# Optimization experiments

Hardware: AMD Instinct MI355X
Metric: run time of the kernel (lower is better)

## Reference

```python
import jax, jax.numpy as jnp
import numpy as np

B, T, I, H, NCLS = 256, 784, 1, 110, 10


def setup_inputs() -> dict:
    key = jax.random.key(0)
    ks = jax.random.split(key, 10)
    s = 1.0 / np.sqrt(H)
    u = lambda k, shape: jax.random.uniform(k, shape, jnp.float32, -s, s)
    return {
        "x": jax.random.normal(ks[0], (B, T, I), jnp.float32),
        "W_ih": u(ks[1], (4 * H, I)),
        "W_hh": u(ks[2], (4 * H, H)),
        "b": u(ks[3], (4 * H,)),
        "W_p": u(ks[4], (1, H)),     # skip-gate readout of cell state
        "b_p": jnp.ones((1,), jnp.float32),  # bias init ~1 -> start by updating
        "h0": u(ks[5], (H,)),        # learned initial hidden (learn_init=True)
        "c0": u(ks[6], (H,)),        # learned initial cell
        "W_fc": u(ks[7], (NCLS, H)),
        "b_fc": u(ks[8], (NCLS,)),
    }


def _st_round(u):
    # straight-through binarization: round in fwd, identity grad in bwd
    return u + jax.lax.stop_gradient(jnp.round(u) - u)


def reference(x, W_ih, W_hh, b, W_p, b_p, h0, c0, W_fc, b_fc):
    Bsz = x.shape[0]
    Hh = h0.shape[0]
    xT = jnp.transpose(x, (1, 0, 2))  # [T, B, I] (the permute in Net.forward)
    h = jnp.broadcast_to(h0, (Bsz, Hh))
    c = jnp.broadcast_to(c0, (Bsz, Hh))
    u0 = jnp.ones((Bsz, 1), x.dtype)  # first step always updates

    def step(carry, xt):
        h, c, u = carry
        ub = _st_round(u)                                  # binary update gate [B,1]
        gates = xt @ W_ih.T + h @ W_hh.T + b               # [B, 4H]
        i, f, g, o = jnp.split(gates, 4, axis=-1)
        i = jax.nn.sigmoid(i)
        f = jax.nn.sigmoid(f)
        o = jax.nn.sigmoid(o)
        g = jnp.tanh(g)
        c_new = f * c + i * g
        h_new = o * jnp.tanh(c_new)
        c_n = ub * c_new + (1.0 - ub) * c                  # skip: keep old state
        h_n = ub * h_new + (1.0 - ub) * h
        du = jax.nn.sigmoid(c_n @ W_p.T + b_p)             # delta-u from cell [B,1]
        u_n = ub * du + (1.0 - ub) * (u + jnp.minimum(du, 1.0 - u))
        return (h_n, c_n, u_n), (h_n, ub)

    (h_last, _, _), (hs, ubs) = jax.lax.scan(step, (h, c, u0), xT)
    out = hs[-1] @ W_fc.T + b_fc                           # fc on last timestep
    total_u = jnp.sum(ubs)                                 # total number of updates
    return out, total_u[None]
```

## Files before the change

### kernel.cpp

```cpp
#include <hip/hip_runtime.h>
#include <stdint.h>


#define T784 784
#define H110 110
#define NT   512
#define NCLS 10
#define LOG2E 1.44269504088896340736f
#define WQS  (0.09535f / 127.0f)

typedef int v4i __attribute__((ext_vector_type(4)));

__device__ __forceinline__ float frcp(float x)  { return __builtin_amdgcn_rcpf(x); }
__device__ __forceinline__ float fexp2(float x) { return __builtin_amdgcn_exp2f(x); }

__device__ __forceinline__ float add_q1(float v) {
    float d; asm("v_add_f32_dpp %0, %1, %1 quad_perm:[1,0,3,2] row_mask:0xf bank_mask:0xf bound_ctrl:0"
                 : "=v"(d) : "v"(v)); return d;
}
__device__ __forceinline__ float add_q2(float v) {
    float d; asm("v_add_f32_dpp %0, %1, %1 quad_perm:[2,3,0,1] row_mask:0xf bank_mask:0xf bound_ctrl:0"
                 : "=v"(d) : "v"(v)); return d;
}
__device__ __forceinline__ float add_hm(float v) {
    float d; asm("v_add_f32_dpp %0, %1, %1 row_half_mirror row_mask:0xf bank_mask:0xf bound_ctrl:0"
                 : "=v"(d) : "v"(v)); return d;
}
__device__ __forceinline__ float add_rm(float v) {
    float d; asm("v_add_f32_dpp %0, %1, %1 row_mirror row_mask:0xf bank_mask:0xf bound_ctrl:0"
                 : "=v"(d) : "v"(v)); return d;
}
__device__ __forceinline__ float add_b15(float v) {
    float d; asm("v_add_f32_dpp %0, %1, %1 row_bcast:15 row_mask:0xf bank_mask:0xf bound_ctrl:0"
                 : "=v"(d) : "v"(v)); return d;
}
__device__ __forceinline__ float add_b31(float v) {
    float d; asm("v_add_f32_dpp %0, %1, %1 row_bcast:31 row_mask:0xf bank_mask:0xf bound_ctrl:0"
                 : "=v"(d) : "v"(v)); return d;
}
template <int L>
__device__ __forceinline__ float qbcast(float v) {
    float d;
    if (L == 0) asm("v_mov_b32_dpp %0, %1 quad_perm:[0,0,0,0] row_mask:0xf bank_mask:0xf bound_ctrl:0" : "=v"(d) : "v"(v));
    if (L == 1) asm("v_mov_b32_dpp %0, %1 quad_perm:[1,1,1,1] row_mask:0xf bank_mask:0xf bound_ctrl:0" : "=v"(d) : "v"(v));
    if (L == 2) asm("v_mov_b32_dpp %0, %1 quad_perm:[2,2,2,2] row_mask:0xf bank_mask:0xf bound_ctrl:0" : "=v"(d) : "v"(v));
    if (L == 3) asm("v_mov_b32_dpp %0, %1 quad_perm:[3,3,3,3] row_mask:0xf bank_mask:0xf bound_ctrl:0" : "=v"(d) : "v"(v));
    return d;
}

__device__ __forceinline__ int qpack(float f0, float f1, float f2, float f3) {
    const int q0 = (int)rintf(f0) & 0xFF;
    const int q1 = (int)rintf(f1) & 0xFF;
    const int q2 = (int)rintf(f2) & 0xFF;
    const int q3 = (int)rintf(f3) & 0xFF;
    return q0 | (q1 << 8) | (q2 << 16) | (q3 << 24);
}

__device__ __forceinline__ int vsel4(v4i a, bool r1, bool r2) {
    const int e01 = r1 ? a[1] : a[0];
    const int e23 = r1 ? a[3] : a[2];
    return r2 ? e23 : e01;
}

__global__ __launch_bounds__(NT, 2)
void skiplstm_kernel(const float* __restrict__ x,
                     const float* __restrict__ W_ih,
                     const float* __restrict__ W_hh,
                     const float* __restrict__ b,
                     const float* __restrict__ W_p,
                     const float* __restrict__ b_p,
                     const float* __restrict__ h0,
                     const float* __restrict__ c0,
                     const float* __restrict__ W_fc,
                     const float* __restrict__ b_fc,
                     float* __restrict__ out)
{
    __shared__ __align__(16) int s_h8[2][32];
    __shared__ float s_pbuf[256];
    __shared__ float s_x[T784];

    const int tid  = threadIdx.x;
    const int bb   = blockIdx.x;
    const int lane = tid & 63;
    const int wid  = tid >> 6;
    const int grp  = lane >> 4;
    const int c    = lane & 15;
    const int q    = tid >> 2;
    const int j    = tid & 3;
    const bool qact = (q < H110);

    const bool i1 = (lane & 4) != 0;
    const bool i2 = (lane & 8) != 0;

    const float qinv = 1.0f / WQS;
    const int  ut  = 16 * wid + c;
    const bool uta = (ut < H110);
    v4i aw[4][2];
    #pragma unroll
    for (int t = 0; t < 4; ++t) {
        const float* rp = W_hh + (t * H110 + ut) * H110;
        #pragma unroll
        for (int kk = 0; kk < 2; ++kk) {
            #pragma unroll
            for (int d = 0; d < 4; ++d) {
                float f[4];
                #pragma unroll
                for (int e = 0; e < 4; ++e) {
                    const int k = kk * 64 + grp * 16 + 4 * d + e;
                    f[e] = (uta && k < H110) ? rp[k] * qinv : 0.0f;
                }
                aw[t][kk][d] = qpack(f[0], f[1], f[2], f[3]);
            }
        }
    }

    const float gfac = (j == 2) ? (-2.0f * LOG2E) : (-LOG2E);
    const int   row  = j * H110 + q;
    const float bv = qact ? b[row]    * gfac : 0.0f;
    const float wv = qact ? W_ih[row] * gfac : 0.0f;
    const float scj = (WQS / 127.0f) * gfac;

    float creg = qact ? c0[q] : 0.0f;
    float hreg = qact ? h0[q] : 0.0f;
    const float wpn = qact ? (-LOG2E) * W_p[q] : 0.0f;
    const float bpn = (-LOG2E) * b_p[0];

    const float mulc = (j == 2) ? 2.0f : 1.0f;
    const float addc = (j == 2) ? -1.0f : 0.0f;

    const v4i z4 = {0, 0, 0, 0};

    for (int i = tid; i < 64;   i += NT) ((int*)s_h8)[i] = 0;
    for (int i = tid; i < 256;  i += NT) s_pbuf[i] = 0.0f;
    for (int i = tid; i < T784; i += NT) s_x[i] = x[bb * T784 + i];
    __syncthreads();
    if (tid < H110)
        ((int8_t*)s_h8[0])[tid] = (int8_t)__float2int_rn(h0[tid] * 127.0f);
    __syncthreads();

    float u_prev = 1.0f;
    int   cnt    = 0;

    auto step = [&](const int* hb, int* hn,
                    const float* pp, float* pn, int t, bool first) {
        const v4i bh0 = ((const v4i*)hb)[grp];
        const v4i bh1 = ((const v4i*)hb)[grp + 4];

        v4i acc0 = __builtin_amdgcn_mfma_i32_16x16x64_i8(aw[0][0], bh0, z4, 0, 0, 0);
        v4i acc1 = __builtin_amdgcn_mfma_i32_16x16x64_i8(aw[1][0], bh0, z4, 0, 0, 0);
        v4i acc2 = __builtin_amdgcn_mfma_i32_16x16x64_i8(aw[2][0], bh0, z4, 0, 0, 0);
        v4i acc3 = __builtin_amdgcn_mfma_i32_16x16x64_i8(aw[3][0], bh0, z4, 0, 0, 0);
        acc0 = __builtin_amdgcn_mfma_i32_16x16x64_i8(aw[0][1], bh1, acc0, 0, 0, 0);
        acc1 = __builtin_amdgcn_mfma_i32_16x16x64_i8(aw[1][1], bh1, acc1, 0, 0, 0);
        acc2 = __builtin_amdgcn_mfma_i32_16x16x64_i8(aw[2][1], bh1, acc2, 0, 0, 0);
        acc3 = __builtin_amdgcn_mfma_i32_16x16x64_i8(aw[3][1], bh1, acc3, 0, 0, 0);

        __builtin_amdgcn_sched_barrier(0);

        const float p0 = pp[lane], p1 = pp[lane + 64];
        const float xt = s_x[t];
        float u_now;
        if (first) {
            u_now = 1.0f;
        } else {
            float v = p0 + p1;
            v = add_q1(v); v = add_q2(v); v = add_hm(v);
            v = add_rm(v); v = add_b15(v); v = add_b31(v);
            const float tot = __int_as_float(
                __builtin_amdgcn_readlane(__float_as_int(v), 63));
            const float du = frcp(1.0f + fexp2(tot + bpn));
            u_now = (u_prev > 0.5f) ? du
                                    : (u_prev + fminf(du, 1.0f - u_prev));
        }
        const bool up = u_now > 0.5f;
        cnt += up ? 1 : 0;
        u_prev = u_now;

        const int e0 = vsel4(acc0, i1, i2);
        const int e1 = vsel4(acc1, i1, i2);
        const int e2 = vsel4(acc2, i1, i2);
        const int e3 = vsel4(acc3, i1, i2);
        const int e01 = (j & 1) ? e1 : e0;
        const int e23 = (j & 1) ? e3 : e2;
        const int ia  = (j & 2) ? e23 : e01;

        const float asel = fmaf((float)ia, scj, fmaf(xt, wv, bv));
        const float av = fmaf(mulc, frcp(1.0f + fexp2(asel)), addc);
        const float gi = qbcast<0>(av);
        const float gf = qbcast<1>(av);
        const float gg = qbcast<2>(av);
        const float go = qbcast<3>(av);

        const float cn = fmaf(gf, creg, gi * gg);
        const float th = fmaf(2.0f, frcp(1.0f + fexp2(cn * (-2.0f * LOG2E))), -1.0f);
        const float hn_ = go * th;
        creg = up ? cn : creg;
        hreg = up ? hn_ : hreg;
        if (qact && j == 0) {
            ((int8_t*)hn)[q] = (int8_t)__float2int_rn(hreg * 127.0f);
            pn[q] = creg * wpn;
        }
        __syncthreads();
    };

    int* const h0b = s_h8[0];
    int* const h1b = s_h8[1];
    float* const p0b = s_pbuf;
    float* const p1b = s_pbuf + 128;

    step(h0b, h1b, p0b, p1b, 0, true);
    step(h1b, h0b, p1b, p0b, 1, false);
    step(h0b, h1b, p0b, p1b, 2, false);
    step(h1b, h0b, p1b, p0b, 3, false);
    for (int t = 4; t < T784; t += 4) {
        step(h0b, h1b, p0b, p1b, t,     false);
        step(h1b, h0b, p1b, p0b, t + 1, false);
        step(h0b, h1b, p0b, p1b, t + 2, false);
        step(h1b, h0b, p1b, p0b, t + 3, false);
    }

    if (qact && j == 0) s_pbuf[q] = hreg;
    __syncthreads();
    if (tid < NCLS) {
        float acc = b_fc[tid];
        for (int k = 0; k < H110; ++k)
            acc = fmaf(s_pbuf[k], W_fc[tid * H110 + k], acc);
        out[bb * NCLS + tid] = acc;
    }
    if (tid == 0)
        atomicAdd(out + 256 * NCLS, (float)cnt);
}

__global__ void zero_tail_kernel(float* out) {
    if (threadIdx.x == 0) out[256 * NCLS] = 0.0f;
}

extern "C" void kernel_launch(void* const* d_in, const int* in_sizes, int n_in,
                              void* d_out, int out_size, void* d_ws, size_t ws_size,
                              hipStream_t stream) {
    const float* x    = (const float*)d_in[0];
    const float* W_ih = (const float*)d_in[1];
    const float* W_hh = (const float*)d_in[2];
    const float* b    = (const float*)d_in[3];
    const float* W_p  = (const float*)d_in[4];
    const float* b_p  = (const float*)d_in[5];
    const float* h0   = (const float*)d_in[6];
    const float* c0   = (const float*)d_in[7];
    const float* W_fc = (const float*)d_in[8];
    const float* b_fc = (const float*)d_in[9];
    float* out = (float*)d_out;

    zero_tail_kernel<<<1, 64, 0, stream>>>(out);
    skiplstm_kernel<<<256, NT, 0, stream>>>(x, W_ih, W_hh, b, W_p, b_p,
                                            h0, c0, W_fc, b_fc, out);
}
```

Before: 406.4 us.

## Halve block size so each thread computes two hidden units per step

Shrinks the workgroup from 8 to 4 waves, and each wave now issues MFMAs for two 64-row groups of hidden units (A and B halves). The gate activations, cell and hidden updates are duplicated per thread for the two units. The goal is to cut the per-timestep cost of the block-wide barrier and cross-wave coordination in this latency-bound recurrence, since fewer waves have to meet each step. In exchange, each wave carries twice the MFMA and transcendental work per step on the critical path and holds twice the weight registers.

```diff
diff --git a/kernel.cpp b/kernel.cpp
--- a/kernel.cpp
+++ b/kernel.cpp
@@ -4,7 +4,7 @@
 
 #define T784 784
 #define H110 110
-#define NT   512
+#define NT   256
 #define NCLS 10
 #define LOG2E 1.44269504088896340736f
 #define WQS  (0.09535f / 127.0f)
@@ -62,7 +62,7 @@
     return r2 ? e23 : e01;
 }
 
-__global__ __launch_bounds__(NT, 2)
+__global__ __launch_bounds__(NT, 1)
 void skiplstm_kernel(const float* __restrict__ x,
                      const float* __restrict__ W_ih,
                      const float* __restrict__ W_hh,
@@ -85,45 +85,55 @@
     const int wid  = tid >> 6;
     const int grp  = lane >> 4;
     const int c    = lane & 15;
-    const int q    = tid >> 2;
     const int j    = tid & 3;
-    const bool qact = (q < H110);
+    const int qA   = tid >> 2;
+    const int qB   = qA + 64;
+    const bool qactB = (qB < H110);
 
     const bool i1 = (lane & 4) != 0;
     const bool i2 = (lane & 8) != 0;
 
     const float qinv = 1.0f / WQS;
-    const int  ut  = 16 * wid + c;
-    const bool uta = (ut < H110);
-    v4i aw[4][2];
+    v4i aw[2][4][2];
     #pragma unroll
-    for (int t = 0; t < 4; ++t) {
-        const float* rp = W_hh + (t * H110 + ut) * H110;
+    for (int g = 0; g < 2; ++g) {
+        const int  ut  = 64 * g + 16 * wid + c;
+        const bool uta = (ut < H110);
         #pragma unroll
-        for (int kk = 0; kk < 2; ++kk) {
+        for (int t = 0; t < 4; ++t) {
+            const float* rp = W_hh + (t * H110 + ut) * H110;
             #pragma unroll
-            for (int d = 0; d < 4; ++d) {
-                float f[4];
+            for (int kk = 0; kk < 2; ++kk) {
                 #pragma unroll
-                for (int e = 0; e < 4; ++e) {
-                    const int k = kk * 64 + grp * 16 + 4 * d + e;
-                    f[e] = (uta && k < H110) ? rp[k] * qinv : 0.0f;
+                for (int d = 0; d < 4; ++d) {
+                    float f[4];
+                    #pragma unroll
+                    for (int e = 0; e < 4; ++e) {
+                        const int k = kk * 64 + grp * 16 + 4 * d + e;
+                        f[e] = (uta && k < H110) ? rp[k] * qinv : 0.0f;
+                    }
+                    aw[g][t][kk][d] = qpack(f[0], f[1], f[2], f[3]);
                 }
-                aw[t][kk][d] = qpack(f[0], f[1], f[2], f[3]);
             }
         }
     }
 
     const float gfac = (j == 2) ? (-2.0f * LOG2E) : (-LOG2E);
-    const int   row  = j * H110 + q;
-    const float bv = qact ? b[row]    * gfac : 0.0f;
-    const float wv = qact ? W_ih[row] * gfac : 0.0f;
-    const float scj = (WQS / 127.0f) * gfac;
-
-    float creg = qact ? c0[q] : 0.0f;
-    float hreg = qact ? h0[q] : 0.0f;
-    const float wpn = qact ? (-LOG2E) * W_p[q] : 0.0f;
-    const float bpn = (-LOG2E) * b_p[0];
+    const float scj  = (WQS / 127.0f) * gfac;
+    const int  rowA  = j * H110 + qA;
+    const int  rowB  = j * H110 + qB;
+    const float bvA = b[rowA]    * gfac;
+    const float wvA = W_ih[rowA] * gfac;
+    const float bvB = qactB ? b[rowB]    * gfac : 0.0f;
+    const float wvB = qactB ? W_ih[rowB] * gfac : 0.0f;
+
+    float cregA = c0[qA];
+    float hregA = h0[qA];
+    float cregB = qactB ? c0[qB] : 0.0f;
+    float hregB = qactB ? h0[qB] : 0.0f;
+    const float wpnA = (-LOG2E) * W_p[qA];
+    const float wpnB = qactB ? (-LOG2E) * W_p[qB] : 0.0f;
+    const float bpn  = (-LOG2E) * b_p[0];
 
     const float mulc = (j == 2) ? 2.0f : 1.0f;
     const float addc = (j == 2) ? -1.0f : 0.0f;
@@ -146,14 +156,22 @@
         const v4i bh0 = ((const v4i*)hb)[grp];
         const v4i bh1 = ((const v4i*)hb)[grp + 4];
 
-        v4i acc0 = __builtin_amdgcn_mfma_i32_16x16x64_i8(aw[0][0], bh0, z4, 0, 0, 0);
-        v4i acc1 = __builtin_amdgcn_mfma_i32_16x16x64_i8(aw[1][0], bh0, z4, 0, 0, 0);
-        v4i acc2 = __builtin_amdgcn_mfma_i32_16x16x64_i8(aw[2][0], bh0, z4, 0, 0, 0);
-        v4i acc3 = __builtin_amdgcn_mfma_i32_16x16x64_i8(aw[3][0], bh0, z4, 0, 0, 0);
-        acc0 = __builtin_amdgcn_mfma_i32_16x16x64_i8(aw[0][1], bh1, acc0, 0, 0, 0);
-        acc1 = __builtin_amdgcn_mfma_i32_16x16x64_i8(aw[1][1], bh1, acc1, 0, 0, 0);
-        acc2 = __builtin_amdgcn_mfma_i32_16x16x64_i8(aw[2][1], bh1, acc2, 0, 0, 0);
-        acc3 = __builtin_amdgcn_mfma_i32_16x16x64_i8(aw[3][1], bh1, acc3, 0, 0, 0);
+        v4i a00 = __builtin_amdgcn_mfma_i32_16x16x64_i8(aw[0][0][0], bh0, z4, 0, 0, 0);
+        v4i a01 = __builtin_amdgcn_mfma_i32_16x16x64_i8(aw[0][1][0], bh0, z4, 0, 0, 0);
+        v4i a02 = __builtin_amdgcn_mfma_i32_16x16x64_i8(aw[0][2][0], bh0, z4, 0, 0, 0);
+        v4i a03 = __builtin_amdgcn_mfma_i32_16x16x64_i8(aw[0][3][0], bh0, z4, 0, 0, 0);
+        v4i a10 = __builtin_amdgcn_mfma_i32_16x16x64_i8(aw[1][0][0], bh0, z4, 0, 0, 0);
+        v4i a11 = __builtin_amdgcn_mfma_i32_16x16x64_i8(aw[1][1][0], bh0, z4, 0, 0, 0);
+        v4i a12 = __builtin_amdgcn_mfma_i32_16x16x64_i8(aw[1][2][0], bh0, z4, 0, 0, 0);
+        v4i a13 = __builtin_amdgcn_mfma_i32_16x16x64_i8(aw[1][3][0], bh0, z4, 0, 0, 0);
+        a00 = __builtin_amdgcn_mfma_i32_16x16x64_i8(aw[0][0][1], bh1, a00, 0, 0, 0);
+        a01 = __builtin_amdgcn_mfma_i32_16x16x64_i8(aw[0][1][1], bh1, a01, 0, 0, 0);
+        a02 = __builtin_amdgcn_mfma_i32_16x16x64_i8(aw[0][2][1], bh1, a02, 0, 0, 0);
+        a03 = __builtin_amdgcn_mfma_i32_16x16x64_i8(aw[0][3][1], bh1, a03, 0, 0, 0);
+        a10 = __builtin_amdgcn_mfma_i32_16x16x64_i8(aw[1][0][1], bh1, a10, 0, 0, 0);
+        a11 = __builtin_amdgcn_mfma_i32_16x16x64_i8(aw[1][1][1], bh1, a11, 0, 0, 0);
+        a12 = __builtin_amdgcn_mfma_i32_16x16x64_i8(aw[1][2][1], bh1, a12, 0, 0, 0);
+        a13 = __builtin_amdgcn_mfma_i32_16x16x64_i8(aw[1][3][1], bh1, a13, 0, 0, 0);
 
         __builtin_amdgcn_sched_barrier(0);
 
@@ -176,29 +194,51 @@
         cnt += up ? 1 : 0;
         u_prev = u_now;
 
-        const int e0 = vsel4(acc0, i1, i2);
-        const int e1 = vsel4(acc1, i1, i2);
-        const int e2 = vsel4(acc2, i1, i2);
-        const int e3 = vsel4(acc3, i1, i2);
-        const int e01 = (j & 1) ? e1 : e0;
-        const int e23 = (j & 1) ? e3 : e2;
-        const int ia  = (j & 2) ? e23 : e01;
-
-        const float asel = fmaf((float)ia, scj, fmaf(xt, wv, bv));
-        const float av = fmaf(mulc, frcp(1.0f + fexp2(asel)), addc);
-        const float gi = qbcast<0>(av);
-        const float gf = qbcast<1>(av);
-        const float gg = qbcast<2>(av);
-        const float go = qbcast<3>(av);
-
-        const float cn = fmaf(gf, creg, gi * gg);
-        const float th = fmaf(2.0f, frcp(1.0f + fexp2(cn * (-2.0f * LOG2E))), -1.0f);
-        const float hn_ = go * th;
-        creg = up ? cn : creg;
-        hreg = up ? hn_ : hreg;
-        if (qact && j == 0) {
-            ((int8_t*)hn)[q] = (int8_t)__float2int_rn(hreg * 127.0f);
-            pn[q] = creg * wpn;
+        const int e00 = vsel4(a00, i1, i2);
+        const int e01s = vsel4(a01, i1, i2);
+        const int e02 = vsel4(a02, i1, i2);
+        const int e03 = vsel4(a03, i1, i2);
+        const int eA01 = (j & 1) ? e01s : e00;
+        const int eA23 = (j & 1) ? e03  : e02;
+        const int iaA  = (j & 2) ? eA23 : eA01;
+        const int e10 = vsel4(a10, i1, i2);
+        const int e11 = vsel4(a11, i1, i2);
+        const int e12 = vsel4(a12, i1, i2);
+        const int e13 = vsel4(a13, i1, i2);
+        const int eB01 = (j & 1) ? e11 : e10;
+        const int eB23 = (j & 1) ? e13 : e12;
+        const int iaB  = (j & 2) ? eB23 : eB01;
+
+        const float aselA = fmaf((float)iaA, scj, fmaf(xt, wvA, bvA));
+        const float aselB = fmaf((float)iaB, scj, fmaf(xt, wvB, bvB));
+        const float avA = fmaf(mulc, frcp(1.0f + fexp2(aselA)), addc);
+        const float avB = fmaf(mulc, frcp(1.0f + fexp2(aselB)), addc);
+        const float giA = qbcast<0>(avA);
+        const float gfA = qbcast<1>(avA);
+        const float ggA = qbcast<2>(avA);
+        const float goA = qbcast<3>(avA);
+        const float giB = qbcast<0>(avB);
+        const float gfB = qbcast<1>(avB);
+        const float ggB = qbcast<2>(avB);
+        const float goB = qbcast<3>(avB);
+
+        const float cnA = fmaf(gfA, cregA, giA * ggA);
+        const float cnB = fmaf(gfB, cregB, giB * ggB);
+        const float thA = fmaf(2.0f, frcp(1.0f + fexp2(cnA * (-2.0f * LOG2E))), -1.0f);
+        const float thB = fmaf(2.0f, frcp(1.0f + fexp2(cnB * (-2.0f * LOG2E))), -1.0f);
+        const float hnA = goA * thA;
+        const float hnB = goB * thB;
+        cregA = up ? cnA : cregA;
+        hregA = up ? hnA : hregA;
+        cregB = up ? cnB : cregB;
+        hregB = up ? hnB : hregB;
+        if (j == 0) {
+            ((int8_t*)hn)[qA] = (int8_t)__float2int_rn(hregA * 127.0f);
+            pn[qA] = cregA * wpnA;
+            if (qactB) {
+                ((int8_t*)hn)[qB] = (int8_t)__float2int_rn(hregB * 127.0f);
+                pn[qB] = cregB * wpnB;
+            }
         }
         __syncthreads();
     };
@@ -219,7 +259,10 @@
         step(h1b, h0b, p1b, p0b, t + 3, false);
     }
 
-    if (qact && j == 0) s_pbuf[q] = hreg;
+    if (j == 0) {
+        s_pbuf[qA] = hregA;
+        if (qactB) s_pbuf[qB] = hregB;
+    }
     __syncthreads();
     if (tid < NCLS) {
         float acc = b_fc[tid];
```

New measurement: 540.6 us. 33.0% more time.
